# Kernel optimization log

Hardware: AMD Instinct MI355X
Metric: run time of the kernel (lower is better)

Reference implementation:

```python
import jax, jax.numpy as jnp
import numpy as np

B, T, C = 4, 1024, 1024
H, D = 16, 64


def setup_inputs() -> dict:
    key = jax.random.key(0)
    ks = jax.random.split(key, 5)
    sc = 0.02
    x = jax.random.normal(ks[0], (B, T, C), dtype=jnp.float32)
    Wq = jax.random.normal(ks[1], (H, C, D), dtype=jnp.float32) * sc
    Wk = jax.random.normal(ks[2], (H, C, D), dtype=jnp.float32) * sc
    Wv = jax.random.normal(ks[3], (H, C, D), dtype=jnp.float32) * sc
    Wp = jax.random.normal(ks[4], (H * D, C), dtype=jnp.float32) * sc
    bp = jnp.zeros((C,), dtype=jnp.float32)
    return {"x": x, "Wq": Wq, "Wk": Wk, "Wv": Wv, "Wp": Wp, "bp": bp}


def reference(x, Wq, Wk, Wv, Wp, bp):
    # per-head projections (bias-free, as in nanoGPT Head)
    q = jnp.einsum('btc,hcd->bhtd', x, Wq)
    k = jnp.einsum('btc,hcd->bhtd', x, Wk)
    v = jnp.einsum('btc,hcd->bhtd', x, Wv)
    scale = 1.0 / jnp.sqrt(jnp.asarray(D, dtype=x.dtype))
    scores = jnp.einsum('bhtd,bhsd->bhts', q, k) * scale  # [B,H,T,T]
    causal = jnp.tril(jnp.ones((T, T), dtype=bool))
    scores = jnp.where(causal, scores, jnp.asarray(-jnp.inf, dtype=scores.dtype))
    attn = jax.nn.softmax(scores, axis=-1)
    out = jnp.einsum('bhts,bhsd->bhtd', attn, v)  # [B,H,T,D]
    out = out.transpose(0, 2, 1, 3).reshape(B, T, H * D)  # concat heads
    return out @ Wp + bp  # final projection (dropout=0)
```

## Files before the change

### kernel.cpp

```cpp
#include <hip/hip_runtime.h>
#include <hip/hip_bf16.h>

typedef unsigned short u16;
typedef __bf16 bf16x8 __attribute__((ext_vector_type(8)));
typedef float floatx4 __attribute__((ext_vector_type(4)));

#define SB 4
#define ST 1024
#define SC 1024
#define SH 16
#define SD 64

__device__ __forceinline__ u16 f2bf(float f) {
    unsigned int u = __builtin_bit_cast(unsigned int, f);
    u += 0x7fffu + ((u >> 16) & 1u);
    return (u16)(u >> 16);
}

__device__ __forceinline__ void gload16(const u16* g, u16* l) {
    __builtin_amdgcn_global_load_lds(
        (const __attribute__((address_space(1))) unsigned int*)g,
        (__attribute__((address_space(3))) unsigned int*)l, 16, 0, 0);
}

__global__ void k_prep(const float* __restrict__ x,
                       const float* __restrict__ Wq, const float* __restrict__ Wk,
                       const float* __restrict__ Wv, const float* __restrict__ Wp,
                       u16* __restrict__ xb, u16* __restrict__ Wqkv, u16* __restrict__ Wpt) {
    __shared__ float tile[64 * 65];
    const int id = blockIdx.x, tid = threadIdx.x;
    if (id < 4096) {
        int i = id * 256 + tid;
        float4 v = ((const float4*)x)[i];
        uint2 o;
        o.x = (unsigned)f2bf(v.x) | ((unsigned)f2bf(v.y) << 16);
        o.y = (unsigned)f2bf(v.z) | ((unsigned)f2bf(v.w) << 16);
        ((uint2*)xb)[i] = o;
    } else if (id < 4864) {
        const int id1 = id - 4096;
        const int qkv = id1 >> 8, rem = id1 & 255, h = rem >> 4, c0 = (rem & 15) * 64;
        const float* src = qkv == 0 ? Wq : (qkv == 1 ? Wk : Wv);
        #pragma unroll
        for (int i = 0; i < 16; ++i) {
            int idx = tid + i * 256;
            int r = idx >> 6, d = idx & 63;
            tile[r * 65 + d] = src[(h * SC + c0 + r) * SD + d];
        }
        __syncthreads();
        #pragma unroll
        for (int i = 0; i < 16; ++i) {
            int idx = tid + i * 256;
            int d = idx >> 6, cc = idx & 63;
            Wqkv[(qkv * 1024 + h * SD + d) * SC + c0 + cc] = f2bf(tile[cc * 65 + d]);
        }
    } else {
        const int id2 = id - 4864;
        const int n0 = (id2 & 15) * 64, k0 = (id2 >> 4) * 64;
        #pragma unroll
        for (int i = 0; i < 16; ++i) {
            int idx = tid + i * 256;
            int r = idx >> 6, nn = idx & 63;
            tile[r * 65 + nn] = Wp[(k0 + r) * SC + n0 + nn];
        }
        __syncthreads();
        #pragma unroll
        for (int i = 0; i < 16; ++i) {
            int idx = tid + i * 256;
            int nr = idx >> 6, kk = idx & 63;
            Wpt[(n0 + nr) * (SH * SD) + k0 + kk] = f2bf(tile[kk * 65 + nr]);
        }
    }
}

__launch_bounds__(256)
__global__ void k_gemm(const u16* __restrict__ A, const u16* __restrict__ Bt,
                       int M, int N, int K,
                       u16* __restrict__ Qb, u16* __restrict__ Kb, u16* __restrict__ Vt) {
    constexpr int BM = 128, BN = 64, SM = 4, SN = 2;
    __shared__ u16 Als[2][BM * 64];
    __shared__ u16 Bls[2][BN * 64];
    const int tid = threadIdx.x, lane = tid & 63, w = tid >> 6;
    const int quad = lane >> 4, l16 = lane & 15;
    const int sr = lane >> 3, sc = lane & 7;
    const int nt = N / BN;
    const int m0 = (blockIdx.x / nt) * BM, n0 = (blockIdx.x % nt) * BN;
    const int wm = (w >> 1) * 64, wn = (w & 1) * 32;

    auto stage = [&](int buf, int k0) {
        #pragma unroll
        for (int i = 0; i < 4; ++i) {
            int rb = (w * 4 + i) * 8;
            gload16(&A[(long)(m0 + rb + sr) * K + k0 + ((sc ^ sr) << 3)], &Als[buf][rb * 64]);
        }
        #pragma unroll
        for (int i = 0; i < 2; ++i) {
            int rb = (w * 2 + i) * 8;
            gload16(&Bt[(long)(n0 + rb + sr) * K + k0 + ((sc ^ sr) << 3)], &Bls[buf][rb * 64]);
        }
    };

    floatx4 acc[SM][SN] = {};
    const int niter = K / 64;
    stage(0, 0);
    for (int it = 0; it < niter; ++it) {
        const int buf = it & 1;
        __syncthreads();
        if (it + 1 < niter) stage(buf ^ 1, (it + 1) * 64);
        bf16x8 af[SM][2], bfr[SN][2];
        #pragma unroll
        for (int sm = 0; sm < SM; ++sm) {
            int row = wm + sm * 16 + l16;
            #pragma unroll
            for (int ks = 0; ks < 2; ++ks)
                af[sm][ks] = *(const bf16x8*)&Als[buf][row * 64 + (((ks * 4 + quad) ^ (row & 7)) << 3)];
        }
        #pragma unroll
        for (int sn = 0; sn < SN; ++sn) {
            int row = wn + sn * 16 + l16;
            #pragma unroll
            for (int ks = 0; ks < 2; ++ks)
                bfr[sn][ks] = *(const bf16x8*)&Bls[buf][row * 64 + (((ks * 4 + quad) ^ (row & 7)) << 3)];
        }
        #pragma unroll
        for (int ks = 0; ks < 2; ++ks)
            #pragma unroll
            for (int sm = 0; sm < SM; ++sm)
                #pragma unroll
                for (int sn = 0; sn < SN; ++sn)
                    acc[sm][sn] = __builtin_amdgcn_mfma_f32_16x16x32_bf16(bfr[sn][ks], af[sm][ks], acc[sm][sn], 0, 0, 0);
    }
    const int qkv = n0 >> 10, h = (n0 & 1023) >> 6;
    const float qs = qkv == 0 ? 0.18033688011112042f : 1.0f;
    #pragma unroll
    for (int sm = 0; sm < SM; ++sm) {
        const int m = m0 + wm + sm * 16 + l16;
        const int bb = m >> 10, t = m & 1023;
        #pragma unroll
        for (int sn = 0; sn < SN; ++sn) {
            const int d0 = wn + sn * 16 + (quad << 2);
            u16 pk[4];
            #pragma unroll
            for (int r = 0; r < 4; ++r) pk[r] = f2bf(acc[sm][sn][r] * qs);
            if (qkv == 2) {
                const long vb = (long)(bb * SH + h) * SD * ST + t;
                #pragma unroll
                for (int r = 0; r < 4; ++r) Vt[vb + (long)(d0 + r) * ST] = pk[r];
            } else {
                u16* dst = qkv == 0 ? Qb : Kb;
                *(uint2*)&dst[(((long)(bb * SH + h) * ST + t) << 6) + d0] = *(uint2*)pk;
            }
        }
    }
}

__launch_bounds__(256)
__global__ void k_oproj(const u16* __restrict__ A, const u16* __restrict__ Bt,
                        const float* __restrict__ bias, float* __restrict__ Cout) {
    constexpr int K = 1024, N = 1024;
    __shared__ u16 Als[4][64 * 64];
    __shared__ u16 Bls[4][64 * 64];
    const int tid = threadIdx.x, lane = tid & 63, w = tid >> 6;
    const int quad = lane >> 4, l16 = lane & 15;
    const int sr = lane >> 3, sc = lane & 7;
    const int m0 = (blockIdx.x >> 4) * 64, n0 = (blockIdx.x & 15) * 64;
    const int wm = (w >> 1) * 32, wn = (w & 1) * 32;

    floatx4 acc[2][2] = {};
    for (int kb = 0; kb < 4; ++kb) {
        const int k0 = kb * 256;
        #pragma unroll
        for (int seg = 0; seg < 4; ++seg) {
            #pragma unroll
            for (int i = 0; i < 2; ++i) {
                int rb = (w * 2 + i) * 8;
                gload16(&A[(long)(m0 + rb + sr) * K + k0 + seg * 64 + ((sc ^ sr) << 3)], &Als[seg][rb * 64]);
                gload16(&Bt[(long)(n0 + rb + sr) * K + k0 + seg * 64 + ((sc ^ sr) << 3)], &Bls[seg][rb * 64]);
            }
        }
        __syncthreads();
        #pragma unroll
        for (int seg = 0; seg < 4; ++seg) {
            bf16x8 af[2][2], bfr[2][2];
            #pragma unroll
            for (int sm = 0; sm < 2; ++sm) {
                int row = wm + sm * 16 + l16;
                #pragma unroll
                for (int ks = 0; ks < 2; ++ks)
                    af[sm][ks] = *(const bf16x8*)&Als[seg][row * 64 + (((ks * 4 + quad) ^ (row & 7)) << 3)];
            }
            #pragma unroll
            for (int sn = 0; sn < 2; ++sn) {
                int row = wn + sn * 16 + l16;
                #pragma unroll
                for (int ks = 0; ks < 2; ++ks)
                    bfr[sn][ks] = *(const bf16x8*)&Bls[seg][row * 64 + (((ks * 4 + quad) ^ (row & 7)) << 3)];
            }
            #pragma unroll
            for (int ks = 0; ks < 2; ++ks)
                #pragma unroll
                for (int sm = 0; sm < 2; ++sm)
                    #pragma unroll
                    for (int sn = 0; sn < 2; ++sn)
                        acc[sm][sn] = __builtin_amdgcn_mfma_f32_16x16x32_bf16(bfr[sn][ks], af[sm][ks], acc[sm][sn], 0, 0, 0);
        }
        if (kb < 3) __syncthreads();
    }
    #pragma unroll
    for (int sn = 0; sn < 2; ++sn) {
        const int nb = n0 + wn + sn * 16 + (quad << 2);
        const float4 bv = *(const float4*)&bias[nb];
        #pragma unroll
        for (int sm = 0; sm < 2; ++sm) {
            const int m = m0 + wm + sm * 16 + l16;
            float4 o;
            o.x = acc[sm][sn][0] + bv.x;
            o.y = acc[sm][sn][1] + bv.y;
            o.z = acc[sm][sn][2] + bv.z;
            o.w = acc[sm][sn][3] + bv.w;
            *(float4*)&Cout[(long)m * N + nb] = o;
        }
    }
}

__launch_bounds__(256)
__global__ void k_attn(const u16* __restrict__ Qg, const u16* __restrict__ Kg,
                       const u16* __restrict__ Vtg, u16* __restrict__ Og) {
    __shared__ u16 Kls[2][64 * 64];
    __shared__ u16 Vls[2][64 * 64];
    __shared__ u16 Pls[64 * 64];
    const int tid = threadIdx.x, lane = tid & 63, w = tid >> 6;
    const int quad = lane >> 4, l16 = lane & 15;
    const int sr = lane >> 3, sc = lane & 7;
    const int tile = 15 - (blockIdx.x >> 6);
    const int bh = blockIdx.x & 63;
    const int t0 = tile * 64;
    const int b = bh >> 4, h = bh & 15;
    const u16* Qbh = Qg + (long)bh * ST * SD;
    const u16* Kbh = Kg + (long)bh * ST * SD;
    const u16* Vbh = Vtg + (long)bh * SD * ST;

    bf16x8 qf[2];
    {
        const u16* qrow = Qbh + (t0 + w * 16 + l16) * SD;
        qf[0] = *(const bf16x8*)&qrow[quad * 8];
        qf[1] = *(const bf16x8*)&qrow[32 + quad * 8];
    }
    floatx4 oacc[4] = {};
    float lsum = 0.f;
    const int myt = t0 + w * 16 + l16;
    const int rowP = w * 16 + l16;

    auto stage = [&](int buf, int s0) {
        #pragma unroll
        for (int i = 0; i < 2; ++i) {
            int rb = (w * 2 + i) * 8;
            gload16(&Kbh[(s0 + rb + sr) * SD + ((sc ^ sr) << 3)], &Kls[buf][rb * 64]);
            gload16(&Vbh[(rb + sr) * ST + s0 + ((sc ^ sr) << 3)], &Vls[buf][rb * 64]);
        }
    };

    stage(0, 0);
    for (int j = 0; j <= tile; ++j) {
        const int buf = j & 1;
        const int s0 = j * 64;
        __syncthreads();
        if (j < tile) stage(buf ^ 1, s0 + 64);

        floatx4 sa[4] = {};
        #pragma unroll
        for (int sn = 0; sn < 4; ++sn) {
            int row = sn * 16 + l16;
            #pragma unroll
            for (int ks = 0; ks < 2; ++ks) {
                bf16x8 kf = *(const bf16x8*)&Kls[buf][row * 64 + (((ks * 4 + quad) ^ (row & 7)) << 3)];
                sa[sn] = __builtin_amdgcn_mfma_f32_16x16x32_bf16(kf, qf[ks], sa[sn], 0, 0, 0);
            }
        }
        const bool diag = (j == tile);
        #pragma unroll
        for (int sn = 0; sn < 4; ++sn) {
            const int sl = sn * 16 + (quad << 2);
            u16 pk[4];
            #pragma unroll
            for (int r = 0; r < 4; ++r) {
                float e = __builtin_exp2f(sa[sn][r]);
                if (diag && s0 + sl + r > myt) e = 0.f;
                lsum += e;
                pk[r] = (u16)(__builtin_bit_cast(unsigned int, e) >> 16);
            }
            *(uint2*)&Pls[rowP * 64 + (((sl >> 3) ^ (rowP & 7)) << 3) + ((quad & 1) << 2)] = *(uint2*)pk;
        }
        bf16x8 pf[2];
        #pragma unroll
        for (int ks = 0; ks < 2; ++ks)
            pf[ks] = *(const bf16x8*)&Pls[rowP * 64 + (((ks * 4 + quad) ^ (rowP & 7)) << 3)];
        #pragma unroll
        for (int dn = 0; dn < 4; ++dn) {
            int row = dn * 16 + l16;
            #pragma unroll
            for (int ks = 0; ks < 2; ++ks) {
                bf16x8 vf = *(const bf16x8*)&Vls[buf][row * 64 + (((ks * 4 + quad) ^ (row & 7)) << 3)];
                oacc[dn] = __builtin_amdgcn_mfma_f32_16x16x32_bf16(vf, pf[ks], oacc[dn], 0, 0, 0);
            }
        }
    }
    float l = lsum;
    l += __shfl_xor(l, 16);
    l += __shfl_xor(l, 32);
    const float inv = 1.0f / l;
    const long obase = ((long)(b * ST + myt) << 10) + h * SD;
    #pragma unroll
    for (int dn = 0; dn < 4; ++dn) {
        u16 pk[4];
        #pragma unroll
        for (int r = 0; r < 4; ++r) pk[r] = f2bf(oacc[dn][r] * inv);
        *(uint2*)&Og[obase + dn * 16 + (quad << 2)] = *(uint2*)pk;
    }
}

extern "C" void kernel_launch(void* const* d_in, const int* in_sizes, int n_in,
                              void* d_out, int out_size, void* d_ws, size_t ws_size,
                              hipStream_t stream) {
    const float* x  = (const float*)d_in[0];
    const float* Wq = (const float*)d_in[1];
    const float* Wk = (const float*)d_in[2];
    const float* Wv = (const float*)d_in[3];
    const float* Wp = (const float*)d_in[4];
    const float* bp = (const float*)d_in[5];
    float* out = (float*)d_out;

    char* ws = (char*)d_ws;
    u16* xb   = (u16*)(ws);
    u16* Wqkv = (u16*)(ws + (8ll  << 20));
    u16* Wpt  = (u16*)(ws + (14ll << 20));
    u16* Qb   = (u16*)(ws + (16ll << 20));
    u16* Kb   = (u16*)(ws + (24ll << 20));
    u16* Vt   = (u16*)(ws + (32ll << 20));
    u16* Ob   = (u16*)(ws + (40ll << 20));

    k_prep<<<5120, 256, 0, stream>>>(x, Wq, Wk, Wv, Wp, xb, Wqkv, Wpt);
    k_gemm<<<32 * 48, 256, 0, stream>>>(xb, Wqkv, 4096, 3072, 1024, Qb, Kb, Vt);
    k_attn<<<1024, 256, 0, stream>>>(Qb, Kb, Vt, Ob);
    k_oproj<<<1024, 256, 0, stream>>>(Ob, Wpt, bp, out);
}
```

Measured before the change: 158.2 us.

## Enlarge GEMM tiles to 128x128 and double-buffer the output projection

The QKV GEMM tile grows from 128x64 to 128x128, so each wave computes a 64x64 sub-tile and the epilogue now derives head and dim per column. The output projection is rebuilt from 64x64 tiles with four-segment bulk loads into a 128x128 tile with a double-buffered K loop like the QKV GEMM. The aim is more operand reuse per LDS load and fewer blocks re-reading the same rows. The cost is more accumulator registers per thread and fewer blocks: 768 for QKV and 256 for the projection, which may underfill the CUs on the projection.

```diff
diff --git a/kernel.cpp b/kernel.cpp
--- a/kernel.cpp
+++ b/kernel.cpp
@@ -76,7 +76,7 @@
 __global__ void k_gemm(const u16* __restrict__ A, const u16* __restrict__ Bt,
                        int M, int N, int K,
                        u16* __restrict__ Qb, u16* __restrict__ Kb, u16* __restrict__ Vt) {
-    constexpr int BM = 128, BN = 64, SM = 4, SN = 2;
+    constexpr int BM = 128, BN = 128, SM = 4, SN = 4;
     __shared__ u16 Als[2][BM * 64];
     __shared__ u16 Bls[2][BN * 64];
     const int tid = threadIdx.x, lane = tid & 63, w = tid >> 6;
@@ -84,17 +84,13 @@
     const int sr = lane >> 3, sc = lane & 7;
     const int nt = N / BN;
     const int m0 = (blockIdx.x / nt) * BM, n0 = (blockIdx.x % nt) * BN;
-    const int wm = (w >> 1) * 64, wn = (w & 1) * 32;
+    const int wm = (w >> 1) * 64, wn = (w & 1) * 64;
 
     auto stage = [&](int buf, int k0) {
         #pragma unroll
         for (int i = 0; i < 4; ++i) {
             int rb = (w * 4 + i) * 8;
             gload16(&A[(long)(m0 + rb + sr) * K + k0 + ((sc ^ sr) << 3)], &Als[buf][rb * 64]);
-        }
-        #pragma unroll
-        for (int i = 0; i < 2; ++i) {
-            int rb = (w * 2 + i) * 8;
             gload16(&Bt[(long)(n0 + rb + sr) * K + k0 + ((sc ^ sr) << 3)], &Bls[buf][rb * 64]);
         }
     };
@@ -129,7 +125,7 @@
                 for (int sn = 0; sn < SN; ++sn)
                     acc[sm][sn] = __builtin_amdgcn_mfma_f32_16x16x32_bf16(bfr[sn][ks], af[sm][ks], acc[sm][sn], 0, 0, 0);
     }
-    const int qkv = n0 >> 10, h = (n0 & 1023) >> 6;
+    const int qkv = n0 >> 10;
     const float qs = qkv == 0 ? 0.18033688011112042f : 1.0f;
     #pragma unroll
     for (int sm = 0; sm < SM; ++sm) {
@@ -137,7 +133,8 @@
         const int bb = m >> 10, t = m & 1023;
         #pragma unroll
         for (int sn = 0; sn < SN; ++sn) {
-            const int d0 = wn + sn * 16 + (quad << 2);
+            const int dl = (n0 & 1023) + wn + sn * 16 + (quad << 2);
+            const int h = dl >> 6, d0 = dl & 63;
             u16 pk[4];
             #pragma unroll
             for (int r = 0; r < 4; ++r) pk[r] = f2bf(acc[sm][sn][r] * qs);
@@ -156,61 +153,60 @@
 __launch_bounds__(256)
 __global__ void k_oproj(const u16* __restrict__ A, const u16* __restrict__ Bt,
                         const float* __restrict__ bias, float* __restrict__ Cout) {
-    constexpr int K = 1024, N = 1024;
-    __shared__ u16 Als[4][64 * 64];
-    __shared__ u16 Bls[4][64 * 64];
+    constexpr int K = 1024, N = 1024, BM = 128, SM = 4, SN = 4;
+    __shared__ u16 Als[2][BM * 64];
+    __shared__ u16 Bls[2][128 * 64];
     const int tid = threadIdx.x, lane = tid & 63, w = tid >> 6;
     const int quad = lane >> 4, l16 = lane & 15;
     const int sr = lane >> 3, sc = lane & 7;
-    const int m0 = (blockIdx.x >> 4) * 64, n0 = (blockIdx.x & 15) * 64;
-    const int wm = (w >> 1) * 32, wn = (w & 1) * 32;
-
-    floatx4 acc[2][2] = {};
-    for (int kb = 0; kb < 4; ++kb) {
-        const int k0 = kb * 256;
-        #pragma unroll
-        for (int seg = 0; seg < 4; ++seg) {
-            #pragma unroll
-            for (int i = 0; i < 2; ++i) {
-                int rb = (w * 2 + i) * 8;
-                gload16(&A[(long)(m0 + rb + sr) * K + k0 + seg * 64 + ((sc ^ sr) << 3)], &Als[seg][rb * 64]);
-                gload16(&Bt[(long)(n0 + rb + sr) * K + k0 + seg * 64 + ((sc ^ sr) << 3)], &Bls[seg][rb * 64]);
-            }
-        }
-        __syncthreads();
-        #pragma unroll
-        for (int seg = 0; seg < 4; ++seg) {
-            bf16x8 af[2][2], bfr[2][2];
-            #pragma unroll
-            for (int sm = 0; sm < 2; ++sm) {
-                int row = wm + sm * 16 + l16;
+    const int m0 = (blockIdx.x >> 3) * BM, n0 = (blockIdx.x & 7) * 128;
+    const int wm = (w >> 1) * 64, wn = (w & 1) * 64;
+
+    auto stage = [&](int buf, int k0) {
+        #pragma unroll
+        for (int i = 0; i < 4; ++i) {
+            int rb = (w * 4 + i) * 8;
+            gload16(&A[(long)(m0 + rb + sr) * K + k0 + ((sc ^ sr) << 3)], &Als[buf][rb * 64]);
+            gload16(&Bt[(long)(n0 + rb + sr) * K + k0 + ((sc ^ sr) << 3)], &Bls[buf][rb * 64]);
+        }
+    };
+
+    floatx4 acc[SM][SN] = {};
+    const int niter = K / 64;
+    stage(0, 0);
+    for (int it = 0; it < niter; ++it) {
+        const int buf = it & 1;
+        __syncthreads();
+        if (it + 1 < niter) stage(buf ^ 1, (it + 1) * 64);
+        bf16x8 af[SM][2], bfr[SN][2];
+        #pragma unroll
+        for (int sm = 0; sm < SM; ++sm) {
+            int row = wm + sm * 16 + l16;
+            #pragma unroll
+            for (int ks = 0; ks < 2; ++ks)
+                af[sm][ks] = *(const bf16x8*)&Als[buf][row * 64 + (((ks * 4 + quad) ^ (row & 7)) << 3)];
+        }
+        #pragma unroll
+        for (int sn = 0; sn < SN; ++sn) {
+            int row = wn + sn * 16 + l16;
+            #pragma unroll
+            for (int ks = 0; ks < 2; ++ks)
+                bfr[sn][ks] = *(const bf16x8*)&Bls[buf][row * 64 + (((ks * 4 + quad) ^ (row & 7)) << 3)];
+        }
+        #pragma unroll
+        for (int ks = 0; ks < 2; ++ks)
+            #pragma unroll
+            for (int sm = 0; sm < SM; ++sm)
                 #pragma unroll
-                for (int ks = 0; ks < 2; ++ks)
-                    af[sm][ks] = *(const bf16x8*)&Als[seg][row * 64 + (((ks * 4 + quad) ^ (row & 7)) << 3)];
-            }
-            #pragma unroll
-            for (int sn = 0; sn < 2; ++sn) {
-                int row = wn + sn * 16 + l16;
-                #pragma unroll
-                for (int ks = 0; ks < 2; ++ks)
-                    bfr[sn][ks] = *(const bf16x8*)&Bls[seg][row * 64 + (((ks * 4 + quad) ^ (row & 7)) << 3)];
-            }
-            #pragma unroll
-            for (int ks = 0; ks < 2; ++ks)
-                #pragma unroll
-                for (int sm = 0; sm < 2; ++sm)
-                    #pragma unroll
-                    for (int sn = 0; sn < 2; ++sn)
-                        acc[sm][sn] = __builtin_amdgcn_mfma_f32_16x16x32_bf16(bfr[sn][ks], af[sm][ks], acc[sm][sn], 0, 0, 0);
-        }
-        if (kb < 3) __syncthreads();
+                for (int sn = 0; sn < SN; ++sn)
+                    acc[sm][sn] = __builtin_amdgcn_mfma_f32_16x16x32_bf16(bfr[sn][ks], af[sm][ks], acc[sm][sn], 0, 0, 0);
     }
     #pragma unroll
-    for (int sn = 0; sn < 2; ++sn) {
+    for (int sn = 0; sn < SN; ++sn) {
         const int nb = n0 + wn + sn * 16 + (quad << 2);
         const float4 bv = *(const float4*)&bias[nb];
         #pragma unroll
-        for (int sm = 0; sm < 2; ++sm) {
+        for (int sm = 0; sm < SM; ++sm) {
             const int m = m0 + wm + sm * 16 + l16;
             float4 o;
             o.x = acc[sm][sn][0] + bv.x;
@@ -339,7 +335,7 @@
     u16* Ob   = (u16*)(ws + (40ll << 20));
 
     k_prep<<<5120, 256, 0, stream>>>(x, Wq, Wk, Wv, Wp, xb, Wqkv, Wpt);
-    k_gemm<<<32 * 48, 256, 0, stream>>>(xb, Wqkv, 4096, 3072, 1024, Qb, Kb, Vt);
+    k_gemm<<<32 * 24, 256, 0, stream>>>(xb, Wqkv, 4096, 3072, 1024, Qb, Kb, Vt);
     k_attn<<<1024, 256, 0, stream>>>(Qb, Kb, Vt, Ob);
-    k_oproj<<<1024, 256, 0, stream>>>(Ob, Wpt, bp, out);
-}
+    k_oproj<<<256, 256, 0, stream>>>(Ob, Wpt, bp, out);
+}
```

Result: slower. 170.6 us (+7.9%).
